# Kernel tuning notes

Hardware: AMD Instinct MI355X
Metric: run time of the kernel (lower is better)

The kernel has to match this reference:

```python
import jax, jax.numpy as jnp
import numpy as np

B, S, E, H = 2, 2048, 1024, 16
HD = E // H            # 64
LAMBDA_INIT = 0.8
EPS = 1e-6


def setup_inputs() -> dict:
    key = jax.random.key(0)
    ks = jax.random.split(key, 8)
    return {
        "x": jax.random.normal(ks[0], (B, S, E), dtype=jnp.float32),
        "w_qkv": jax.random.normal(ks[1], (E, 3 * E), dtype=jnp.float32) * (E ** -0.5),
        "wo": jax.random.normal(ks[2], (E, E), dtype=jnp.float32) * (E ** -0.5),
        "lambda_q1": jax.random.normal(ks[3], (HD,), dtype=jnp.float32) * 0.1,
        "lambda_q2": jax.random.normal(ks[4], (HD,), dtype=jnp.float32) * 0.1,
        "lambda_k1": jax.random.normal(ks[5], (HD,), dtype=jnp.float32) * 0.1,
        "lambda_k2": jax.random.normal(ks[6], (HD,), dtype=jnp.float32) * 0.1,
        "norm_w": jnp.ones((H, HD), dtype=jnp.float32),
    }


def reference(x, w_qkv, wo, lambda_q1, lambda_q2, lambda_k1, lambda_k2, norm_w):
    b, s, e = x.shape
    qkv = x @ w_qkv                                   # [b, s, 3e]
    q, k, v = jnp.split(qkv, 3, axis=-1)
    def to_heads(t):
        return t.reshape(b, s, H, HD).transpose(0, 2, 1, 3)  # [b, H, s, hd]
    q, k, v = to_heads(q), to_heads(k), to_heads(v)
    q1, q2 = jnp.split(q, 2, axis=-1)                 # [b, H, s, hd/2]
    k1, k2 = jnp.split(k, 2, axis=-1)
    scale = 1.0 / jnp.sqrt(jnp.asarray(HD, dtype=x.dtype))  # note: full head_dim, as in source
    a1 = jax.nn.softmax(jnp.einsum('bhsd,bhtd->bhst', q1, k1) * scale, axis=-1)
    a2 = jax.nn.softmax(jnp.einsum('bhsd,bhtd->bhst', q2, k2) * scale, axis=-1)
    lam = jnp.exp(jnp.dot(lambda_q1, lambda_k1)) - jnp.exp(jnp.dot(lambda_q2, lambda_k2)) + LAMBDA_INIT
    a = a1 - lam * a2                                 # [b, H, s, s]
    out = jnp.einsum('bhst,bhtd->bhsd', a, v)         # [b, H, s, hd]
    # per-head RMSNorm, scaled by (1 - lambda_init)
    rms = jnp.sqrt(jnp.mean(out * out, axis=-1, keepdims=True) + EPS)
    out_n = (out / rms) * norm_w[None, :, None, :] * (1.0 - LAMBDA_INIT)
    # replicate source's cat(dim=1) -> transpose(1,2) -> view(b, s, e)
    out_cat = out_n.reshape(b, H * s, HD)             # concat of per-head [b, s, hd]
    out_final = out_cat.transpose(0, 2, 1).reshape(b, s, e)
    return out_final @ wo
```

## Files before the change

### kernel.cpp

```cpp
#include <hip/hip_runtime.h>
#include <math.h>

#define B_ 2
#define S_ 2048
#define E_ 1024
#define H_ 16
#define HD_ 64
#define LAMBDA_INIT 0.8f
#define EPS_ 1e-6f

typedef __attribute__((ext_vector_type(8))) short short8;
typedef __attribute__((ext_vector_type(8))) unsigned short ushort8v;
typedef __attribute__((ext_vector_type(4))) float floatx4;
typedef __attribute__((ext_vector_type(16))) float floatx16;

__device__ __forceinline__ unsigned short f2bf(float f) {
  unsigned u = __float_as_uint(f);
  u += 0x7FFFu + ((u >> 16) & 1u);
  return (unsigned short)(u >> 16);
}

__device__ __forceinline__ void gl_lds16(const void* g, void* l) {
  __builtin_amdgcn_global_load_lds((const __attribute__((address_space(1))) void*)g,
                                   (__attribute__((address_space(3))) void*)l,
                                   16, 0, 0);
}

__global__ __launch_bounds__(256) void prep(const float* __restrict__ x,
                                            const float* __restrict__ w_qkv,
                                            const float* __restrict__ wo,
                                            unsigned short* __restrict__ xB,
                                            unsigned short* __restrict__ WT,
                                            unsigned short* __restrict__ woT) {
  __shared__ float tile[64][65];
  const int tid = threadIdx.x;
  const int bid = blockIdx.x;
  if (bid < 1024) {
    const int n4 = 4096 * 1024 / 4;
    for (int i = bid * 256 + tid; i < n4; i += 1024 * 256) {
      float4 v = ((const float4*)x)[i];
      ushort4 w;
      w.x = f2bf(v.x); w.y = f2bf(v.y); w.z = f2bf(v.z); w.w = f2bf(v.w);
      ((ushort4*)xB)[i] = w;
    }
    return;
  }
  const float* in;
  unsigned short* out;
  int R, C, bx, by;
  if (bid < 1792) {
    in = w_qkv; out = WT; R = 1024; C = 3072;
    int t = bid - 1024; bx = t % 48; by = t / 48;
  } else {
    in = wo; out = woT; R = 1024; C = 1024;
    int t = bid - 1792; bx = t % 16; by = t / 16;
  }
  const int c0 = bx * 64;
  const int r0 = by * 64;
#pragma unroll
  for (int it = 0; it < 16; it++) {
    int e = tid + it * 256;
    int rr = e >> 6, cc = e & 63;
    tile[rr][cc] = in[(size_t)(r0 + rr) * C + c0 + cc];
  }
  __syncthreads();
#pragma unroll
  for (int it = 0; it < 16; it++) {
    int e = tid + it * 256;
    int rr = e >> 6, cc = e & 63;
    out[(size_t)(c0 + rr) * R + r0 + cc] = f2bf(tile[cc][rr]);
  }
}

template <bool BF16OUT, int BNT>
__device__ __forceinline__ void gemm_body(unsigned short* AsB, unsigned short* BsB,
                                          const unsigned short* __restrict__ A,
                                          const unsigned short* __restrict__ Bt,
                                          void* __restrict__ C, int M, int N, int K,
                                          int bx, int by) {
  const int tid = threadIdx.x;
  const int wave = tid >> 6, lane = tid & 63;
  const int lane15 = lane & 15, quad = lane >> 4;
  const int m0 = by * 128;
  const int n0 = bx * BNT;
  const int wm = (wave & 1) * 64, wn = (wave >> 1) * (BNT / 2);
  const int NI = BNT / 32;

  floatx4 acc[4][NI];
#pragma unroll
  for (int mi = 0; mi < 4; mi++)
#pragma unroll
    for (int ni = 0; ni < NI; ni++) acc[mi][ni] = (floatx4)0.0f;

  const int rsA = wave * 32 + (lane >> 3);
  const int rsB = wave * (BNT / 4) + (lane >> 3);
  const int cph = lane & 7;

#define GSTAGE(k0_, As_, Bs_)                                                  \
  {                                                                            \
    _Pragma("unroll")                                                          \
    for (int j = 0; j < 4; j++) {                                              \
      int r = rsA + j * 8;                                                     \
      int cl = cph ^ (r & 7);                                                  \
      gl_lds16(A + (size_t)(m0 + r) * K + (k0_) + cl * 8,                      \
               (As_) + (wave * 32 + j * 8) * 64);                              \
    }                                                                          \
    _Pragma("unroll")                                                          \
    for (int j = 0; j < BNT / 32; j++) {                                       \
      int r = rsB + j * 8;                                                     \
      int cl = cph ^ (r & 7);                                                  \
      gl_lds16(Bt + (size_t)(n0 + r) * K + (k0_) + cl * 8,                     \
               (Bs_) + (wave * (BNT / 4) + j * 8) * 64);                       \
    }                                                                          \
  }

  GSTAGE(0, AsB, BsB);
  __syncthreads();

  int cur = 0;
  for (int k0 = 0; k0 < K; k0 += 64) {
    if (k0 + 64 < K)
      GSTAGE(k0 + 64, AsB + (cur ^ 1) * (128 * 64), BsB + (cur ^ 1) * (BNT * 64));
    const unsigned short* As = AsB + cur * (128 * 64);
    const unsigned short* Bs = BsB + cur * (BNT * 64);

#pragma unroll
    for (int ks = 0; ks < 2; ks++) {
      short8 af[4], bf[NI];
#pragma unroll
      for (int mi = 0; mi < 4; mi++) {
        int r = wm + mi * 16 + lane15;
        int phys = (ks * 4 + quad) ^ (r & 7);
        af[mi] = *(const short8*)(&As[r * 64 + phys * 8]);
      }
#pragma unroll
      for (int ni = 0; ni < NI; ni++) {
        int r = wn + ni * 16 + lane15;
        int phys = (ks * 4 + quad) ^ (r & 7);
        bf[ni] = *(const short8*)(&Bs[r * 64 + phys * 8]);
      }
#pragma unroll
      for (int mi = 0; mi < 4; mi++)
#pragma unroll
        for (int ni = 0; ni < NI; ni++)
          acc[mi][ni] = __builtin_amdgcn_mfma_f32_16x16x32_bf16(af[mi], bf[ni],
                                                                acc[mi][ni], 0, 0, 0);
    }
    __syncthreads();
    cur ^= 1;
  }
#undef GSTAGE

#pragma unroll
  for (int mi = 0; mi < 4; mi++)
#pragma unroll
    for (int ni = 0; ni < NI; ni++)
#pragma unroll
      for (int reg = 0; reg < 4; reg++) {
        int row = m0 + wm + mi * 16 + quad * 4 + reg;
        int col = n0 + wn + ni * 16 + lane15;
        float v = acc[mi][ni][reg];
        if (BF16OUT)
          ((unsigned short*)C)[(size_t)row * N + col] = f2bf(v);
        else
          ((float*)C)[(size_t)row * N + col] = v;
      }
}

template <bool BF16OUT, int BNT>
__global__ __launch_bounds__(256, BNT == 64 ? 2 : 1) void gemm_bt(
    const unsigned short* __restrict__ A, const unsigned short* __restrict__ Bt,
    void* __restrict__ C, int M, int N, int K) {
  __shared__ __align__(16) unsigned short As[2 * 128 * 64];
  __shared__ __align__(16) unsigned short Bs[2 * BNT * 64];
  gemm_body<BF16OUT, BNT>(As, Bs, A, Bt, C, M, N, K, blockIdx.x, blockIdx.y);
}

__global__ __launch_bounds__(256) void qkv_gemm(const unsigned short* __restrict__ xB,
                                                const unsigned short* __restrict__ WT,
                                                unsigned short* __restrict__ qkB,
                                                unsigned short* __restrict__ vTB) {
  __shared__ __align__(16) unsigned short As[2 * 128 * 64];
  __shared__ __align__(16) unsigned short Bs[2 * 128 * 64];
  const int id = blockIdx.x;
  if (id < 512) {
    gemm_body<true, 128>(As, Bs, xB, WT, qkB, 4096, 2048, 1024, id & 15, id >> 4);
  } else {
    const int t = id - 512;
    gemm_body<true, 64>(As, Bs, WT + (size_t)2048 * 1024, xB, vTB, 1024, 4096, 1024,
                        t & 63, t >> 6);
  }
}

__global__ __launch_bounds__(512, 4) void flash_attn_mfma(
    const unsigned short* __restrict__ qkB, const unsigned short* __restrict__ vTB,
    const float* __restrict__ lq1, const float* __restrict__ lq2,
    const float* __restrict__ lk1, const float* __restrict__ lk2,
    const float* __restrict__ norm_w, unsigned short* __restrict__ hid) {
  __shared__ __align__(16) unsigned short KV[2][2][64 * 64];
  __shared__ float Lex[4][64];
  __shared__ float LF2[64][130];

  const int tid = threadIdx.x;
  const int wave = tid >> 6, lane = tid & 63;
  const int l31 = lane & 31, hi = lane >> 5;
  const int qsub = wave >> 1, sw = wave & 1;

  const int bid = (blockIdx.x & 7) * 64 + (blockIdx.x >> 3);
  const int qt = bid & 15;
  const int h = (bid >> 4) & 15;
  const int b = bid >> 8;
  const int q0 = qt * 128;

  float a1 = 0.f, a2 = 0.f;
  for (int d = 0; d < HD_; d++) {
    a1 += lq1[d] * lk1[d];
    a2 += lq2[d] * lk2[d];
  }
  const float lam = __expf(a1) - __expf(a2) + LAMBDA_INIT;

  short8 qf[2];
  {
    const unsigned short* qrow =
        qkB + (size_t)(b * S_ + q0 + qsub * 32 + l31) * 2048 + h * 64 + sw * 32;
#pragma unroll
    for (int cs = 0; cs < 2; cs++)
      qf[cs] = *(const short8*)(qrow + cs * 16 + hi * 8);
  }

  floatx16 accO[2];
#pragma unroll
  for (int n = 0; n < 2; n++) accO[n] = (floatx16)0.0f;
  float lsum = 0.f;
  const floatx16 zero16 = (floatx16)0.0f;

  const int srow = tid >> 3;
  const int scol = tid & 7;
  const size_t kgbase = (size_t)(b * S_) * 2048 + 1024 + h * 64;
  const size_t vgbase = (size_t)h * 64 * 4096 + b * 2048;

#define STAGE(t_, buf_)                                                        \
  {                                                                            \
    const size_t kg_ = kgbase + (size_t)(t_) * 64 * 2048;                      \
    const size_t vg_ = vgbase + (size_t)(t_) * 64;                             \
    const int cl_ = scol ^ (srow & 7);                                         \
    gl_lds16(qkB + kg_ + (size_t)srow * 2048 + cl_ * 8,                        \
             &KV[buf_][0][(wave * 8) * 64]);                                   \
    gl_lds16(vTB + vg_ + (size_t)srow * 4096 + cl_ * 8,                        \
             &KV[buf_][1][(wave * 8) * 64]);                                   \
  }

  STAGE(0, 0);
  __syncthreads();

  int cur = 0;
  for (int t = 0; t < S_ / 64; t++) {
    if (t < S_ / 64 - 1) STAGE(t + 1, cur ^ 1);
    const unsigned short* Kc = &KV[cur][0][0];
    const unsigned short* Vc = &KV[cur][1][0];

#pragma unroll
    for (int kb = 0; kb < 2; kb++) {
      const int krow = kb * 32 + l31;
      const int kx = krow & 7;
      floatx16 accS = zero16;
#pragma unroll
      for (int cs = 0; cs < 2; cs++) {
        const int pc = (sw * 4 + cs * 2 + hi) ^ kx;
        const short8 kf = *(const short8*)(Kc + krow * 64 + pc * 8);
        accS = __builtin_amdgcn_mfma_f32_32x32x16_bf16(kf, qf[cs], accS, 0, 0, 0);
      }
      unsigned w[8];
      float ls = 0.f;
#pragma unroll
      for (int i = 0; i < 8; i++) {
        float p0 = __expf(accS[2 * i] * 0.125f);
        float p1 = __expf(accS[2 * i + 1] * 0.125f);
        ls += p0 + p1;
        asm("v_cvt_pk_bf16_f32 %0, %1, %2" : "=v"(w[i]) : "v"(p0), "v"(p1));
      }
      lsum += ls;
      asm volatile("v_permlane32_swap_b32 %0, %1" : "+v"(w[0]), "+v"(w[2]));
      asm volatile("v_permlane32_swap_b32 %0, %1" : "+v"(w[1]), "+v"(w[3]));
      asm volatile("v_permlane32_swap_b32 %0, %1" : "+v"(w[4]), "+v"(w[6]));
      asm volatile("v_permlane32_swap_b32 %0, %1" : "+v"(w[5]), "+v"(w[7]));
      uint4 u0 = make_uint4(w[0], w[1], w[2], w[3]);
      uint4 u1 = make_uint4(w[4], w[5], w[6], w[7]);
      short8 pf0 = __builtin_bit_cast(short8, u0);
      short8 pf1 = __builtin_bit_cast(short8, u1);
#pragma unroll
      for (int ks2 = 0; ks2 < 2; ks2++) {
        const short8 pa = ks2 ? pf1 : pf0;
#pragma unroll
        for (int n = 0; n < 2; n++) {
          const int vrow = n * 32 + l31;
          const int pc = (kb * 4 + ks2 * 2 + hi) ^ (vrow & 7);
          const short8 vf = *(const short8*)(Vc + vrow * 64 + pc * 8);
          accO[n] = __builtin_amdgcn_mfma_f32_32x32x16_bf16(pa, vf, accO[n], 0, 0, 0);
        }
      }
    }
    __syncthreads();
    cur ^= 1;
  }
#undef STAGE

  lsum += __shfl_xor(lsum, 32, 64);

  float* LF = (float*)&KV[0][0][0];
  if (sw == 1) {
    Lex[qsub][lane] = lsum;
#pragma unroll
    for (int n = 0; n < 2; n++)
#pragma unroll
      for (int r = 0; r < 16; r++)
        LF[qsub * 2048 + (n * 16 + r) * 64 + lane] = accO[n][r];
  }
  __syncthreads();

  if (sw == 0) {
    const float ls2v = Lex[qsub][lane];
    const float* nw = norm_w + h * HD_;
    const float nw0 = nw[l31], nw1 = nw[32 + l31];
#pragma unroll
    for (int r = 0; r < 16; r++) {
      const int qr = (r & 3) + 8 * (r >> 2) + 4 * hi;
      const float s1 = __shfl(lsum, qr, 64);
      const float s2 = __shfl(ls2v, qr, 64);
      const float inv1 = 1.0f / s1;
      const float c2 = lam / s2;
      const float b0 = LF[qsub * 2048 + (0 * 16 + r) * 64 + lane];
      const float b1 = LF[qsub * 2048 + (1 * 16 + r) * 64 + lane];
      float o0 = accO[0][r] * inv1 - b0 * c2;
      float o1 = accO[1][r] * inv1 - b1 * c2;
      float ss = o0 * o0 + o1 * o1;
#pragma unroll
      for (int msk = 1; msk <= 16; msk <<= 1) ss += __shfl_xor(ss, msk, 64);
      const float rsc = (1.0f - LAMBDA_INIT) * rsqrtf(ss * (1.0f / 64.0f) + EPS_);
      LF2[l31][qsub * 32 + qr] = o0 * rsc * nw0;
      LF2[32 + l31][qsub * 32 + qr] = o1 * rsc * nw1;
    }
  }
  __syncthreads();

  {
    const int d = tid >> 3, g = tid & 7;
    unsigned short* dst =
        hid + (size_t)b * (S_ * E_) + (size_t)d * (H_ * S_) + h * S_ + q0 + g * 16;
    ushort8v v0, v1;
#pragma unroll
    for (int j = 0; j < 8; j++) {
      v0[j] = f2bf(LF2[d][g * 16 + j]);
      v1[j] = f2bf(LF2[d][g * 16 + 8 + j]);
    }
    *(ushort8v*)(dst) = v0;
    *(ushort8v*)(dst + 8) = v1;
  }
}

extern "C" void kernel_launch(void* const* d_in, const int* in_sizes, int n_in,
                              void* d_out, int out_size, void* d_ws, size_t ws_size,
                              hipStream_t stream) {
  const float* x = (const float*)d_in[0];
  const float* w_qkv = (const float*)d_in[1];
  const float* wo = (const float*)d_in[2];
  const float* lq1 = (const float*)d_in[3];
  const float* lq2 = (const float*)d_in[4];
  const float* lk1 = (const float*)d_in[5];
  const float* lk2 = (const float*)d_in[6];
  const float* norm_w = (const float*)d_in[7];
  float* out = (float*)d_out;

  unsigned short* xB = (unsigned short*)d_ws;
  unsigned short* WT = xB + (size_t)4096 * 1024;
  unsigned short* woT = WT + (size_t)3072 * 1024;
  unsigned short* qkB = woT + (size_t)1024 * 1024;
  unsigned short* vTB = qkB + (size_t)4096 * 2048;
  unsigned short* hidB = vTB + (size_t)1024 * 4096;

  prep<<<2048, 256, 0, stream>>>(x, w_qkv, wo, xB, WT, woT);

  qkv_gemm<<<1024, 256, 0, stream>>>(xB, WT, qkB, vTB);

  flash_attn_mfma<<<B_ * H_ * (S_ / 128), 512, 0, stream>>>(qkB, vTB, lq1, lq2, lk1,
                                                            lk2, norm_w, hidB);
  gemm_bt<false, 64><<<dim3(1024 / 64, 4096 / 128), 256, 0, stream>>>(
      hidB, woT, (void*)out, 4096, 1024, 1024);
}
```

Measured before the change: 219.4 us.

## Halve GEMM K-tile to raise occupancy and add MFMA priority hints in attention

The shared GEMM body now stages K in chunks of 32 instead of 64, with a new 4-way XOR swizzle, which halves the LDS footprint per block. The qkv_gemm launch bound is raised to 4 blocks per CU to exploit that. Separately, the flash attention loop wraps its MFMA sections in s_setprio raises so matrix work is favoured over other waves' softmax math. The trade-off is twice as many barriers and K-loop iterations, with less work between syncs to hide global-to-LDS latency.

Measured after the change: 226.9 us. 3.4% more time.

```diff
diff --git a/kernel.cpp b/kernel.cpp
--- a/kernel.cpp
+++ b/kernel.cpp
@@ -85,6 +85,7 @@
   const int n0 = bx * BNT;
   const int wm = (wave & 1) * 64, wn = (wave >> 1) * (BNT / 2);
   const int NI = BNT / 32;
+  const int RB = BNT / 64;
 
   floatx4 acc[4][NI];
 #pragma unroll
@@ -92,25 +93,24 @@
 #pragma unroll
     for (int ni = 0; ni < NI; ni++) acc[mi][ni] = (floatx4)0.0f;
 
-  const int rsA = wave * 32 + (lane >> 3);
-  const int rsB = wave * (BNT / 4) + (lane >> 3);
-  const int cph = lane & 7;
+  const int lrow = lane >> 2;
+  const int cph = lane & 3;
 
 #define GSTAGE(k0_, As_, Bs_)                                                  \
   {                                                                            \
     _Pragma("unroll")                                                          \
-    for (int j = 0; j < 4; j++) {                                              \
-      int r = rsA + j * 8;                                                     \
-      int cl = cph ^ (r & 7);                                                  \
+    for (int j = 0; j < 2; j++) {                                              \
+      int r = wave * 32 + lrow + j * 16;                                       \
+      int cl = cph ^ ((r >> 1) & 3);                                           \
       gl_lds16(A + (size_t)(m0 + r) * K + (k0_) + cl * 8,                      \
-               (As_) + (wave * 32 + j * 8) * 64);                              \
+               (As_) + (wave * 32 + j * 16) * 32);                             \
     }                                                                          \
     _Pragma("unroll")                                                          \
-    for (int j = 0; j < BNT / 32; j++) {                                       \
-      int r = rsB + j * 8;                                                     \
-      int cl = cph ^ (r & 7);                                                  \
+    for (int j = 0; j < RB; j++) {                                             \
+      int r = wave * (BNT / 4) + lrow + j * 16;                                \
+      int cl = cph ^ ((r >> 1) & 3);                                           \
       gl_lds16(Bt + (size_t)(n0 + r) * K + (k0_) + cl * 8,                     \
-               (Bs_) + (wave * (BNT / 4) + j * 8) * 64);                       \
+               (Bs_) + (wave * (BNT / 4) + j * 16) * 32);                      \
     }                                                                          \
   }
 
@@ -118,34 +118,31 @@
   __syncthreads();
 
   int cur = 0;
-  for (int k0 = 0; k0 < K; k0 += 64) {
-    if (k0 + 64 < K)
-      GSTAGE(k0 + 64, AsB + (cur ^ 1) * (128 * 64), BsB + (cur ^ 1) * (BNT * 64));
-    const unsigned short* As = AsB + cur * (128 * 64);
-    const unsigned short* Bs = BsB + cur * (BNT * 64);
-
-#pragma unroll
-    for (int ks = 0; ks < 2; ks++) {
-      short8 af[4], bf[NI];
-#pragma unroll
-      for (int mi = 0; mi < 4; mi++) {
-        int r = wm + mi * 16 + lane15;
-        int phys = (ks * 4 + quad) ^ (r & 7);
-        af[mi] = *(const short8*)(&As[r * 64 + phys * 8]);
-      }
-#pragma unroll
-      for (int ni = 0; ni < NI; ni++) {
-        int r = wn + ni * 16 + lane15;
-        int phys = (ks * 4 + quad) ^ (r & 7);
-        bf[ni] = *(const short8*)(&Bs[r * 64 + phys * 8]);
-      }
-#pragma unroll
-      for (int mi = 0; mi < 4; mi++)
-#pragma unroll
-        for (int ni = 0; ni < NI; ni++)
-          acc[mi][ni] = __builtin_amdgcn_mfma_f32_16x16x32_bf16(af[mi], bf[ni],
-                                                                acc[mi][ni], 0, 0, 0);
-    }
+  for (int k0 = 0; k0 < K; k0 += 32) {
+    if (k0 + 32 < K)
+      GSTAGE(k0 + 32, AsB + (cur ^ 1) * (128 * 32), BsB + (cur ^ 1) * (BNT * 32));
+    const unsigned short* As = AsB + cur * (128 * 32);
+    const unsigned short* Bs = BsB + cur * (BNT * 32);
+
+    short8 af[4], bf[NI];
+#pragma unroll
+    for (int mi = 0; mi < 4; mi++) {
+      int r = wm + mi * 16 + lane15;
+      int phys = quad ^ ((r >> 1) & 3);
+      af[mi] = *(const short8*)(&As[r * 32 + phys * 8]);
+    }
+#pragma unroll
+    for (int ni = 0; ni < NI; ni++) {
+      int r = wn + ni * 16 + lane15;
+      int phys = quad ^ ((r >> 1) & 3);
+      bf[ni] = *(const short8*)(&Bs[r * 32 + phys * 8]);
+    }
+#pragma unroll
+    for (int mi = 0; mi < 4; mi++)
+#pragma unroll
+      for (int ni = 0; ni < NI; ni++)
+        acc[mi][ni] = __builtin_amdgcn_mfma_f32_16x16x32_bf16(af[mi], bf[ni],
+                                                              acc[mi][ni], 0, 0, 0);
     __syncthreads();
     cur ^= 1;
   }
@@ -171,17 +168,16 @@
 __global__ __launch_bounds__(256, BNT == 64 ? 2 : 1) void gemm_bt(
     const unsigned short* __restrict__ A, const unsigned short* __restrict__ Bt,
     void* __restrict__ C, int M, int N, int K) {
-  __shared__ __align__(16) unsigned short As[2 * 128 * 64];
-  __shared__ __align__(16) unsigned short Bs[2 * BNT * 64];
+  __shared__ __align__(16) unsigned short As[2 * 128 * 32];
+  __shared__ __align__(16) unsigned short Bs[2 * BNT * 32];
   gemm_body<BF16OUT, BNT>(As, Bs, A, Bt, C, M, N, K, blockIdx.x, blockIdx.y);
 }
 
-__global__ __launch_bounds__(256) void qkv_gemm(const unsigned short* __restrict__ xB,
-                                                const unsigned short* __restrict__ WT,
-                                                unsigned short* __restrict__ qkB,
-                                                unsigned short* __restrict__ vTB) {
-  __shared__ __align__(16) unsigned short As[2 * 128 * 64];
-  __shared__ __align__(16) unsigned short Bs[2 * 128 * 64];
+__global__ __launch_bounds__(256, 4) void qkv_gemm(
+    const unsigned short* __restrict__ xB, const unsigned short* __restrict__ WT,
+    unsigned short* __restrict__ qkB, unsigned short* __restrict__ vTB) {
+  __shared__ __align__(16) unsigned short As[2 * 128 * 32];
+  __shared__ __align__(16) unsigned short Bs[2 * 128 * 32];
   const int id = blockIdx.x;
   if (id < 512) {
     gemm_body<true, 128>(As, Bs, xB, WT, qkB, 4096, 2048, 1024, id & 15, id >> 4);
@@ -264,12 +260,14 @@
       const int krow = kb * 32 + l31;
       const int kx = krow & 7;
       floatx16 accS = zero16;
+      __builtin_amdgcn_s_setprio(1);
 #pragma unroll
       for (int cs = 0; cs < 2; cs++) {
         const int pc = (sw * 4 + cs * 2 + hi) ^ kx;
         const short8 kf = *(const short8*)(Kc + krow * 64 + pc * 8);
         accS = __builtin_amdgcn_mfma_f32_32x32x16_bf16(kf, qf[cs], accS, 0, 0, 0);
       }
+      __builtin_amdgcn_s_setprio(0);
       unsigned w[8];
       float ls = 0.f;
 #pragma unroll
@@ -288,6 +286,7 @@
       uint4 u1 = make_uint4(w[4], w[5], w[6], w[7]);
       short8 pf0 = __builtin_bit_cast(short8, u0);
       short8 pf1 = __builtin_bit_cast(short8, u1);
+      __builtin_amdgcn_s_setprio(1);
 #pragma unroll
       for (int ks2 = 0; ks2 < 2; ks2++) {
         const short8 pa = ks2 ? pf1 : pf0;
@@ -299,6 +298,7 @@
           accO[n] = __builtin_amdgcn_mfma_f32_32x32x16_bf16(pa, vf, accO[n], 0, 0, 0);
         }
       }
+      __builtin_amdgcn_s_setprio(0);
     }
     __syncthreads();
     cur ^= 1;
```
